# Optimization experiments

Hardware: AMD Instinct MI355X
Metric: run time of the kernel (lower is better)

## Reference

```python
import jax, jax.numpy as jnp
import numpy as np
from jax import lax

B, H, W = 8, 64, 64
D_IN, D_OUT, HEADS = 288, 576, 8
WIN, QS = 16, 2
MLP_H, BOT, NEXP = 4 * D_OUT, 32, 2
HEAD_DIM = D_OUT // HEADS


def _ln(x, g, b, eps=1e-6):
    m = jnp.mean(x, axis=-1, keepdims=True)
    v = jnp.var(x, axis=-1, keepdims=True)
    return (x - m) * lax.rsqrt(v + eps) * g + b


def _max_pool2(x):  # NHWC 2x2 max pool, stride 2
    return lax.reduce_window(x, -jnp.inf, lax.max, (1, 2, 2, 1), (1, 2, 2, 1), 'VALID')


def setup_inputs():
    key = jax.random.key(0)
    ks = iter(jax.random.split(key, 16))
    s = 0.02
    p = {}
    p['rgb'] = jax.random.normal(next(ks), (B, H, W, D_IN), jnp.float32)
    p['depth'] = jax.random.normal(next(ks), (B, H, W, D_IN), jnp.float32)
    p['norm1_g'] = jnp.ones((D_IN,), jnp.float32)
    p['norm1_b'] = jnp.zeros((D_IN,), jnp.float32)
    p['proj_w'] = jax.random.normal(next(ks), (D_IN, D_OUT), jnp.float32) * s
    p['proj_b'] = jnp.zeros((D_OUT,), jnp.float32)
    p['qkv_w'] = jax.random.normal(next(ks), (D_IN, 3 * D_OUT), jnp.float32) * s
    p['qkv_b'] = jnp.zeros((3 * D_OUT,), jnp.float32)
    p['attn_proj_w'] = jax.random.normal(next(ks), (D_OUT, D_OUT), jnp.float32) * s
    p['attn_proj_b'] = jnp.zeros((D_OUT,), jnp.float32)
    p['norm2_g'] = jnp.ones((D_OUT,), jnp.float32)
    p['norm2_b'] = jnp.zeros((D_OUT,), jnp.float32)
    p['mlp_w1'] = jax.random.normal(next(ks), (D_OUT, MLP_H), jnp.float32) * s
    p['mlp_b1'] = jnp.zeros((MLP_H,), jnp.float32)
    p['mlp_w2'] = jax.random.normal(next(ks), (MLP_H, D_OUT), jnp.float32) * s
    p['mlp_b2'] = jnp.zeros((D_OUT,), jnp.float32)
    # per-stream (rgb=0, depth=1) MoE adapters: 2 experts, bottleneck 32
    p['ad_gate_w'] = jax.random.normal(next(ks), (2, D_OUT, NEXP), jnp.float32) * s
    p['ad_gate_b'] = jnp.zeros((2, NEXP), jnp.float32)
    p['ad_down_w'] = jax.random.normal(next(ks), (2, NEXP, D_OUT, BOT), jnp.float32) * s
    p['ad_down_b'] = jnp.zeros((2, NEXP, BOT), jnp.float32)
    p['ad_up_w'] = jax.random.normal(next(ks), (2, NEXP, BOT, D_OUT), jnp.float32) * s
    p['ad_up_b'] = jnp.zeros((2, NEXP, D_OUT), jnp.float32)
    return p


def reference(rgb, depth, norm1_g, norm1_b, proj_w, proj_b, qkv_w, qkv_b,
              attn_proj_w, attn_proj_b, norm2_g, norm2_b,
              mlp_w1, mlp_b1, mlp_w2, mlp_b2,
              ad_gate_w, ad_gate_b, ad_down_w, ad_down_b, ad_up_w, ad_up_b):
    nW = H // WIN  # 4 windows per side (64 divisible by 16, no padding)
    w2 = WIN // QS  # pooled window side = 8

    def adapter(x, si):
        gate = jax.nn.softmax(x @ ad_gate_w[si] + ad_gate_b[si], axis=-1)  # [B,h,w,E]
        h = jax.nn.gelu(jnp.einsum('bhwd,edr->bhwer', x, ad_down_w[si]) + ad_down_b[si])
        y = jnp.einsum('bhwer,erd->bhwed', h, ad_up_w[si]) + ad_up_b[si]
        return 0.5 * jnp.sum(gate[..., None] * y, axis=-2)

    def stream(x, si):
        xn = _ln(x, norm1_g, norm1_b)
        # dim changes -> shortcut = do_pool(proj(norm1(x)))
        shortcut = _max_pool2(xn @ proj_w + proj_b)  # [B,32,32,576]
        xw = xn.reshape(B, nW, WIN, nW, WIN, D_IN).transpose(0, 1, 3, 2, 4, 5)
        xw = xw.reshape(B * nW * nW, WIN, WIN, D_IN)
        Bw = xw.shape[0]
        qkv = (xw.reshape(Bw, WIN * WIN, D_IN) @ qkv_w + qkv_b)
        qkv = qkv.reshape(Bw, WIN * WIN, 3, HEADS, HEAD_DIM)
        q, k, v = qkv[:, :, 0], qkv[:, :, 1], qkv[:, :, 2]
        # q-pool (2x2 max) inside each window
        q = _max_pool2(q.reshape(Bw, WIN, WIN, D_OUT)).reshape(Bw, w2 * w2, HEADS, HEAD_DIM)
        scale = 1.0 / np.sqrt(HEAD_DIM).astype(np.float32)
        attn = jax.nn.softmax(jnp.einsum('bqhd,bkhd->bhqk', q, k) * scale, axis=-1)
        o = jnp.einsum('bhqk,bkhd->bqhd', attn, v).reshape(Bw, w2, w2, D_OUT)
        o = o @ attn_proj_w + attn_proj_b
        # unpartition with pooled window size into 32x32
        o = o.reshape(B, nW, nW, w2, w2, D_OUT).transpose(0, 1, 3, 2, 4, 5)
        o = o.reshape(B, nW * w2, nW * w2, D_OUT)
        x = shortcut + o
        h = _ln(x, norm2_g, norm2_b)
        mlp = jax.nn.gelu(h @ mlp_w1 + mlp_b1) @ mlp_w2 + mlp_b2
        return x + mlp + adapter(x, si)

    return jnp.stack([stream(rgb, 0), stream(depth, 1)])  # [2,B,32,32,576]
```

## Files before the change

kernel.cpp:

```cpp
#include <hip/hip_runtime.h>
#include <cstdint>
#include <math.h>

typedef __bf16 bf16_t;
typedef __bf16 bf16x8 __attribute__((ext_vector_type(8)));
typedef float f32x4 __attribute__((ext_vector_type(4)));
typedef uint32_t u32x4 __attribute__((ext_vector_type(4)));
typedef uint32_t u32x2 __attribute__((ext_vector_type(2)));

#define DI __device__ __forceinline__

DI float bflo(uint32_t u){ return __builtin_bit_cast(float, (uint32_t)(u << 16)); }
DI float bfhi(uint32_t u){ return __builtin_bit_cast(float, (uint32_t)(u & 0xffff0000u)); }
DI uint16_t f2bf(float f){ bf16_t h = (bf16_t)f; return __builtin_bit_cast(uint16_t, h); }
DI uint32_t pk2(float a, float b){ return (uint32_t)f2bf(a) | ((uint32_t)f2bf(b) << 16); }
DI float geluf(float x){
  float u = 0.7978845608028654f * (x + 0.044715f * x * x * x);
  return 0.5f * x * (1.0f + tanhf(u));
}

#if defined(__has_builtin)
#if __has_builtin(__builtin_amdgcn_global_load_lds)
#define USE_GLLDS 1
#endif
#endif

#if USE_GLLDS
DI void gload_lds16(const void* g, void* l){
  __builtin_amdgcn_global_load_lds((__attribute__((address_space(1))) void*)g,
                                   (__attribute__((address_space(3))) void*)l, 16, 0, 0);
}
#endif

__global__ __launch_bounds__(256) void vtpad_k(uint16_t* __restrict__ vt)
{
  int idx = blockIdx.x * 256 + threadIdx.x;
  int wh = idx >> 11, r = (idx >> 8) & 7, c = idx & 255;
  vt[((size_t)(wh * 80 + 72 + r)) * 256 + c] = 0;
}

__global__ __launch_bounds__(256) void wtrans_k(const float* __restrict__ W, uint16_t* __restrict__ Wt,
                                                int K, int N, int Np, int ldw, int c0)
{
  int idx = blockIdx.x * 256 + threadIdx.x;
  if (idx >= Np * K) return;
  int n = idx / K, k = idx - n * K;
  float v = (n < N) ? W[(size_t)k * ldw + c0 + n] : 0.0f;
  Wt[idx] = f2bf(v);
}

__global__ __launch_bounds__(256) void mk_m2te_k(const float* __restrict__ w2,
    const float* __restrict__ uw, const float* __restrict__ ub, uint16_t* __restrict__ m2Te)
{
  int idx = blockIdx.x * 256 + threadIdx.x;
  if (idx >= 2 * 640 * 2400) return;
  int si = idx / (640 * 2400);
  int rem = idx - si * 640 * 2400;
  int n = rem / 2400, k = rem - n * 2400;
  float v = 0.0f;
  if (n < 576){
    if (k < 2304) v = w2[(size_t)k * 576 + n];
    else if (k < 2368){
      int e = (k - 2304) >> 5, r = (k - 2304) & 31;
      v = uw[((size_t)(si * 2 + e) * 32 + r) * 576 + n];
    } else if (k < 2370){
      v = ub[(size_t)(si * 2 + (k - 2368)) * 576 + n];
    }
  }
  m2Te[idx] = f2bf(v);
}

__global__ __launch_bounds__(256) void mk_adt_k(const float* __restrict__ dwn, const float* __restrict__ gw,
    const float* __restrict__ dbn, const float* __restrict__ gb,
    uint16_t* __restrict__ adT, float* __restrict__ adB)
{
  int idx = blockIdx.x * 256 + threadIdx.x;
  if (idx >= 2 * 128 * 576) return;
  int si = idx / (128 * 576);
  int rem = idx - si * 128 * 576;
  int n = rem / 576, k = rem - n * 576;
  float v = 0.0f;
  if (n < 64){
    int e = n >> 5, r = n & 31;
    v = dwn[((size_t)(si * 2 + e) * 576 + k) * 32 + r];
  } else if (n < 66){
    v = gw[(size_t)si * 1152 + k * 2 + (n - 64)];
  }
  adT[idx] = f2bf(v);
  if (k == 0){
    float bv = 0.0f;
    if (n < 64) bv = dbn[si * 64 + (n >> 5) * 32 + (n & 31)];
    else if (n < 66) bv = gb[si * 2 + (n - 64)];
    adB[si * 128 + n] = bv;
  }
}

__global__ __launch_bounds__(256) void mk_pqb_k(const float* __restrict__ pb, const float* __restrict__ qb,
                                                float* __restrict__ o)
{
  int i = blockIdx.x * 256 + threadIdx.x;
  if (i < 1280){
    float v = 0.0f;
    if (i < 576) v = pb[i];
    else if (i >= 640 && i < 1216) v = qb[i - 640];
    o[i] = v;
  }
}

__global__ __launch_bounds__(256) void ln_k(const float* __restrict__ in0, const int D,
                                            const float* __restrict__ g, const float* __restrict__ bb,
                                            uint16_t* __restrict__ outp)
{
  const int token = blockIdx.x * 4 + (threadIdx.x >> 6);
  const int lane = threadIdx.x & 63;
  const float* in = in0 + (size_t)token * D;
  const int nf4 = D >> 2;
  f32x4 v[3];
  float s = 0.f, sq = 0.f;
#pragma unroll
  for (int i = 0; i < 3; ++i){
    const int c = lane + 64 * i;
    if (c < nf4){
      v[i] = *(const f32x4*)(in + 4 * c);
#pragma unroll
      for (int e = 0; e < 4; ++e){ s += v[i][e]; sq += v[i][e] * v[i][e]; }
    }
  }
#pragma unroll
  for (int off = 32; off; off >>= 1){
    s  += __shfl_xor(s, off);
    sq += __shfl_xor(sq, off);
  }
  const float mean = s / (float)D;
  const float var = sq / (float)D - mean * mean;
  const float inv = rsqrtf(var + 1e-6f);
  uint16_t* orow = outp + (size_t)token * D;
#pragma unroll
  for (int i = 0; i < 3; ++i){
    const int c = lane + 64 * i;
    if (c < nf4){
      float f0 = (v[i][0] - mean) * inv * g[4*c+0] + bb[4*c+0];
      float f1 = (v[i][1] - mean) * inv * g[4*c+1] + bb[4*c+1];
      float f2 = (v[i][2] - mean) * inv * g[4*c+2] + bb[4*c+2];
      float f3 = (v[i][3] - mean) * inv * g[4*c+3] + bb[4*c+3];
      u32x2 pk; pk[0] = pk2(f0, f1); pk[1] = pk2(f2, f3);
      *(u32x2*)(orow + 4 * c) = pk;
    }
  }
}

template<int BM>
DI void gemm_core(const uint16_t* __restrict__ A, const uint16_t* __restrict__ Bt,
                  const int K, char* smem, const int tid, f32x4 (*acc)[4])
{
  constexpr int MI = BM / 32;
  constexpr int ABUF = BM * 64;
  char* A0 = smem;
  char* A1 = smem + ABUF;
  char* B0 = smem + 2 * ABUF;
  char* B1 = smem + 2 * ABUF + 8192;
  const int lane = tid & 63;
  const int wid = tid >> 6;
  const int wm = (wid >> 1) * (BM / 2);
  const int wn = (wid & 1) * 64;
  const int r15 = lane & 15, kh = lane >> 4;
  const int rA0 = tid >> 2, c16 = tid & 3;
  const int kS = ((c16 ^ ((rA0 >> 1) & 3)) << 3);

  auto stage = [&](char* Ad, char* Bd, int t){
    const uint16_t* ga0 = A + (size_t)rA0 * K + t * 32 + kS;
    const uint16_t* gb0 = Bt + (size_t)rA0 * K + t * 32 + kS;
    const uint16_t* gb1 = Bt + (size_t)(rA0 + 64) * K + t * 32 + kS;
#if USE_GLLDS
    gload_lds16(ga0, Ad + tid * 16);
    gload_lds16(gb0, Bd + tid * 16);
    gload_lds16(gb1, Bd + tid * 16 + 4096);
    if constexpr (BM == 128){
      const uint16_t* ga1 = A + (size_t)(rA0 + 64) * K + t * 32 + kS;
      gload_lds16(ga1, Ad + tid * 16 + 4096);
    }
#else
    *(u32x4*)(Ad + tid * 16)        = *(const u32x4*)ga0;
    *(u32x4*)(Bd + tid * 16)        = *(const u32x4*)gb0;
    *(u32x4*)(Bd + tid * 16 + 4096) = *(const u32x4*)gb1;
    if constexpr (BM == 128){
      const uint16_t* ga1 = A + (size_t)(rA0 + 64) * K + t * 32 + kS;
      *(u32x4*)(Ad + tid * 16 + 4096) = *(const u32x4*)ga1;
    }
#endif
  };

  stage(A0, B0, 0);
  __syncthreads();
  const int nt = K >> 5;
  for (int t = 0; t < nt; ++t){
    char* Ac = (t & 1) ? A1 : A0;
    char* Bc = (t & 1) ? B1 : B0;
    if (t + 1 < nt) stage((t & 1) ? A0 : A1, (t & 1) ? B0 : B1, t + 1);
    bf16x8 af[MI], bfv[4];
#pragma unroll
    for (int i = 0; i < MI; ++i){
      int rowA = wm + i * 16 + r15;
      af[i] = *(const bf16x8*)(Ac + rowA * 64 + ((kh ^ ((rowA >> 1) & 3)) << 4));
    }
#pragma unroll
    for (int j = 0; j < 4; ++j){
      int rowB = wn + j * 16 + r15;
      bfv[j] = *(const bf16x8*)(Bc + rowB * 64 + ((kh ^ ((rowB >> 1) & 3)) << 4));
    }
#pragma unroll
    for (int i = 0; i < MI; ++i)
#pragma unroll
      for (int j = 0; j < 4; ++j)
        acc[i][j] = __builtin_amdgcn_mfma_f32_16x16x32_bf16(af[i], bfv[j], acc[i][j], 0, 0, 0);
    __syncthreads();
  }
}

__global__ __launch_bounds__(256) void gemm_pkv_k(
    const uint16_t* __restrict__ xn, const uint16_t* __restrict__ pqT, const uint16_t* __restrict__ kvT,
    const float* __restrict__ pqB, const float* __restrict__ kvB,
    uint16_t* __restrict__ sc, uint16_t* __restrict__ qp,
    uint16_t* __restrict__ kb, uint16_t* __restrict__ vt)
{
  __shared__ __align__(16) char smem[32768];
  const int tid = threadIdx.x;
  const int m0 = blockIdx.x * 128;
  const int y = blockIdx.y;
  const bool pool = (y < 10);
  const int n0 = pool ? y * 128 : (y - 10) * 128;
  const uint16_t* Bt = (pool ? pqT : kvT) + (size_t)n0 * 288;
  f32x4 acc[4][4] = {};
  gemm_core<128>(xn + (size_t)m0 * 288, Bt, 288, smem, tid, acc);

  const int lane = tid & 63, wid = tid >> 6;
  const int wm = (wid >> 1) * 64, wn = (wid & 1) * 64;
  const int r15 = lane & 15, kh = lane >> 4;

  if (pool){
    uint16_t* Cp = (uint16_t*)smem;
#pragma unroll
    for (int i = 0; i < 4; ++i)
#pragma unroll
      for (int j = 0; j < 4; ++j)
#pragma unroll
        for (int tt = 0; tt < 4; ++tt){
          int rr2 = wm + i * 16 + kh * 4 + tt;
          int cc = wn + j * 16 + r15;
          Cp[rr2 * 128 + cc] = f2bf(acc[i][j][tt]);
        }
    __syncthreads();
    const int orow0 = m0 >> 2;
#pragma unroll
    for (int e2 = 0; e2 < 16; ++e2){
      int idx = tid + 256 * e2;
      int X = idx >> 7, c = idx & 127;
      int gn = n0 + c;
      if (gn < 1216){
        float v0 = bflo(Cp[(2 * X) * 128 + c]);
        float v1 = bflo(Cp[(2 * X + 1) * 128 + c]);
        float v2 = bflo(Cp[(64 + 2 * X) * 128 + c]);
        float v3 = bflo(Cp[(65 + 2 * X) * 128 + c]);
        float v = fmaxf(fmaxf(v0, v1), fmaxf(v2, v3)) + pqB[gn];
        if (gn < 576)
          sc[(size_t)(orow0 + X) * 576 + gn] = f2bf(v);
        else if (gn >= 640){
          int qn = gn - 640;
          if (qn < 576) qp[(size_t)(orow0 + X) * 576 + qn] = f2bf(v);
        }
      }
    }
  } else {
    int coln[4]; float bcol[4];
#pragma unroll
    for (int j = 0; j < 4; ++j){
      coln[j] = n0 + wn + j * 16 + r15;
      bcol[j] = kvB[coln[j]];
    }
#pragma unroll
    for (int i = 0; i < 4; ++i)
#pragma unroll
      for (int tt = 0; tt < 4; ++tt){
        const int gm = m0 + wm + i * 16 + kh * 4 + tt;
#pragma unroll
        for (int j = 0; j < 4; ++j){
          float v = acc[i][j][tt] + bcol[j];
          int n = coln[j];
          if (n < 576){
            kb[(size_t)gm * 576 + n] = f2bf(v);
          } else {
            int d = n - 576;
            int hh = d / 72, dd = d - hh * 72;
            int bimg = gm >> 12, yy = (gm >> 6) & 63, xx = gm & 63;
            int w = bimg * 16 + (yy >> 4) * 4 + (xx >> 4);
            int kl = (yy & 15) * 16 + (xx & 15);
            vt[((size_t)(w * 8 + hh) * 80 + dd) * 256 + kl] = f2bf(v);
          }
        }
      }
  }
}

__global__ __launch_bounds__(256) void gemm_add1_k(
    const uint16_t* __restrict__ ob, const uint16_t* __restrict__ aT, const float* __restrict__ bias,
    const uint16_t* __restrict__ sc, float* __restrict__ x2, uint16_t* __restrict__ x2b)
{
  __shared__ __align__(16) char smem[24576];
  const int tid = threadIdx.x;
  const int m0 = blockIdx.x * 64;
  const int n0 = blockIdx.y * 128;
  f32x4 acc[2][4] = {};
  gemm_core<64>(ob + (size_t)m0 * 576, aT + (size_t)n0 * 576, 576, smem, tid, acc);

  const int lane = tid & 63, wid = tid >> 6;
  const int wm = (wid >> 1) * 32, wn = (wid & 1) * 64;
  const int r15 = lane & 15, kh = lane >> 4;
  int coln[4]; float bcol[4];
#pragma unroll
  for (int j = 0; j < 4; ++j){
    coln[j] = n0 + wn + j * 16 + r15;
    bcol[j] = (coln[j] < 576) ? bias[coln[j]] : 0.0f;
  }
#pragma unroll
  for (int i = 0; i < 2; ++i)
#pragma unroll
    for (int tt = 0; tt < 4; ++tt){
      const int gm = m0 + wm + i * 16 + kh * 4 + tt;
      const size_t ro = (size_t)gm * 576;
#pragma unroll
      for (int j = 0; j < 4; ++j){
        if (coln[j] < 576){
          float v = acc[i][j][tt] + bcol[j] + bflo(sc[ro + coln[j]]);
          x2[ro + coln[j]] = v;
          x2b[ro + coln[j]] = f2bf(v);
        }
      }
    }
}

__global__ __launch_bounds__(256) void gemm_upad_k(
    const uint16_t* __restrict__ hb, const uint16_t* __restrict__ x2b,
    const uint16_t* __restrict__ m1T, const uint16_t* __restrict__ adT,
    const float* __restrict__ b1, const float* __restrict__ adB,
    uint16_t* __restrict__ mlpA)
{
  __shared__ __align__(16) char smem[24576];
  const int tid = threadIdx.x;
  const int m0 = blockIdx.x * 64;
  const int y = blockIdx.y;
  const bool up = (y < 18);
  const int n0 = up ? y * 128 : 0;
  const uint16_t* A = (up ? hb : x2b) + (size_t)m0 * 576;
  const uint16_t* Bt = up ? (m1T + (size_t)n0 * 576) : adT;
  f32x4 acc[2][4] = {};
  gemm_core<64>(A, Bt, 576, smem, tid, acc);

  const int lane = tid & 63, wid = tid >> 6;
  const int wm = (wid >> 1) * 32, wn = (wid & 1) * 64;
  const int r15 = lane & 15, kh = lane >> 4;

  if (up){
    const float* bias = b1;
#pragma unroll
    for (int i = 0; i < 2; ++i)
#pragma unroll
      for (int tt = 0; tt < 4; ++tt){
        const int gm = m0 + wm + i * 16 + kh * 4 + tt;
#pragma unroll
        for (int j = 0; j < 4; ++j){
          int c = n0 + wn + j * 16 + r15;
          float v = acc[i][j][tt] + bias[c];
          mlpA[(size_t)gm * 2400 + c] = f2bf(geluf(v));
        }
      }
  } else {
    float* gl = (float*)smem;
#pragma unroll
    for (int i = 0; i < 2; ++i)
#pragma unroll
      for (int j = 0; j < 4; ++j){
        int c = wn + j * 16 + r15;
        if (c == 64 || c == 65){
#pragma unroll
          for (int tt = 0; tt < 4; ++tt){
            int rr2 = wm + i * 16 + kh * 4 + tt;
            gl[rr2 * 2 + (c - 64)] = acc[i][j][tt] + adB[c];
          }
        }
      }
    __syncthreads();
#pragma unroll
    for (int i = 0; i < 2; ++i)
#pragma unroll
      for (int tt = 0; tt < 4; ++tt){
        int rr2 = wm + i * 16 + kh * 4 + tt;
        int gm = m0 + rr2;
        float l0 = gl[rr2 * 2], l1 = gl[rr2 * 2 + 1];
        float mx = fmaxf(l0, l1);
        float e0 = __expf(l0 - mx), e1 = __expf(l1 - mx);
        float inv = 0.5f / (e0 + e1);
#pragma unroll
        for (int j = 0; j < 4; ++j){
          int c = wn + j * 16 + r15;
          if (c < 96){
            float val;
            if (c < 64){
              float g = ((c >> 5) == 0 ? e0 : e1) * inv;
              val = g * geluf(acc[i][j][tt] + adB[c]);
            } else if (c == 64) val = e0 * inv;
            else if (c == 65) val = e1 * inv;
            else val = 0.0f;
            mlpA[(size_t)gm * 2400 + 2304 + c] = f2bf(val);
          }
        }
      }
  }
}

__global__ __launch_bounds__(256) void gemm_addf_k(
    const uint16_t* __restrict__ mlpA, const uint16_t* __restrict__ m2Te, const float* __restrict__ bias,
    const float* __restrict__ x2, float* __restrict__ outf)
{
  __shared__ __align__(16) char smem[24576];
  const int tid = threadIdx.x;
  const int m0 = blockIdx.x * 64;
  const int n0 = blockIdx.y * 128;
  f32x4 acc[2][4] = {};
  gemm_core<64>(mlpA + (size_t)m0 * 2400, m2Te + (size_t)n0 * 2400, 2400, smem, tid, acc);

  const int lane = tid & 63, wid = tid >> 6;
  const int wm = (wid >> 1) * 32, wn = (wid & 1) * 64;
  const int r15 = lane & 15, kh = lane >> 4;
  int coln[4]; float bcol[4];
#pragma unroll
  for (int j = 0; j < 4; ++j){
    coln[j] = n0 + wn + j * 16 + r15;
    bcol[j] = (coln[j] < 576) ? bias[coln[j]] : 0.0f;
  }
#pragma unroll
  for (int i = 0; i < 2; ++i)
#pragma unroll
    for (int tt = 0; tt < 4; ++tt){
      const int gm = m0 + wm + i * 16 + kh * 4 + tt;
      const size_t ro = (size_t)gm * 576;
#pragma unroll
      for (int j = 0; j < 4; ++j){
        if (coln[j] < 576){
          float v = acc[i][j][tt] + bcol[j] + x2[ro + coln[j]];
          outf[ro + coln[j]] = v;
        }
      }
    }
}

__global__ __launch_bounds__(64, 1) void attn_mfma_k(
    const uint16_t* __restrict__ qp,
    const uint16_t* __restrict__ kb,
    const uint16_t* __restrict__ vt,
    uint16_t* __restrict__ o)
{
  const int lane = threadIdx.x;
  const int r15 = lane & 15;
  const int kh = lane >> 4;
  const int bid = blockIdx.x;
  const int h = bid & 7;
  const int w = bid >> 3;
  const int b = w >> 4;
  const int wy = (w >> 2) & 3;
  const int wx = w & 3;

  const u32x4 ZU = {0, 0, 0, 0};
  const bf16x8 Z8 = __builtin_bit_cast(bf16x8, ZU);
  const float scale = 0.11785113019775793f;

  bf16x8 qf[4][3];
  int qrow[4];
#pragma unroll
  for (int j = 0; j < 4; ++j){
    int q = j * 16 + r15;
    int y = wy * 8 + (q >> 3), x = wx * 8 + (q & 7);
    qrow[j] = b * 1024 + y * 32 + x;
    const uint16_t* qpr = qp + (size_t)qrow[j] * 576 + h * 72;
    qf[j][0] = *(const bf16x8*)(qpr + kh * 8);
    qf[j][1] = *(const bf16x8*)(qpr + 32 + kh * 8);
    qf[j][2] = (kh == 0) ? *(const bf16x8*)(qpr + 64) : Z8;
  }

  float m[4], l[4];
#pragma unroll
  for (int j = 0; j < 4; ++j){ m[j] = -INFINITY; l[j] = 0.0f; }
  f32x4 acco[5][4] = {};
  const size_t vtbase = (size_t)(w * 8 + h) * 80 * 256;

  for (int t = 0; t < 4; ++t){
    f32x4 accs[4][4] = {};
#pragma unroll
    for (int i = 0; i < 4; ++i){
      const uint16_t* kr = kb + (size_t)(b * 4096 + (wy * 16 + t * 4 + i) * 64 + wx * 16 + r15) * 576 + h * 72;
      bf16x8 kf0 = *(const bf16x8*)(kr + kh * 8);
      bf16x8 kf1 = *(const bf16x8*)(kr + 32 + kh * 8);
      bf16x8 kf2 = (kh == 0) ? *(const bf16x8*)(kr + 64) : Z8;
#pragma unroll
      for (int j = 0; j < 4; ++j){
        accs[i][j] = __builtin_amdgcn_mfma_f32_16x16x32_bf16(kf0, qf[j][0], accs[i][j], 0, 0, 0);
        accs[i][j] = __builtin_amdgcn_mfma_f32_16x16x32_bf16(kf1, qf[j][1], accs[i][j], 0, 0, 0);
        accs[i][j] = __builtin_amdgcn_mfma_f32_16x16x32_bf16(kf2, qf[j][2], accs[i][j], 0, 0, 0);
      }
    }
#pragma unroll
    for (int j = 0; j < 4; ++j){
      float mx = -INFINITY;
#pragma unroll
      for (int i = 0; i < 4; ++i)
#pragma unroll
        for (int tt = 0; tt < 4; ++tt){
          float sv = accs[i][j][tt] * scale;
          accs[i][j][tt] = sv;
          mx = fmaxf(mx, sv);
        }
      mx = fmaxf(mx, __shfl_xor(mx, 16));
      mx = fmaxf(mx, __shfl_xor(mx, 32));
      float nm = fmaxf(m[j], mx);
      float f = __expf(m[j] - nm);
      m[j] = nm;
      l[j] *= f;
#pragma unroll
      for (int i2 = 0; i2 < 5; ++i2) acco[i2][j] *= f;
      float ls = 0.0f;
#pragma unroll
      for (int i = 0; i < 4; ++i)
#pragma unroll
        for (int tt = 0; tt < 4; ++tt){
          float p = __expf(accs[i][j][tt] - nm);
          accs[i][j][tt] = p;
          ls += p;
        }
      ls += __shfl_xor(ls, 16);
      ls += __shfl_xor(ls, 32);
      l[j] += ls;
    }
    uint32_t pw[4][4][2];
#pragma unroll
    for (int i = 0; i < 4; ++i)
#pragma unroll
      for (int j = 0; j < 4; ++j){
        pw[i][j][0] = pk2(accs[i][j][0], accs[i][j][1]);
        pw[i][j][1] = pk2(accs[i][j][2], accs[i][j][3]);
      }
#pragma unroll
    for (int ks = 0; ks < 2; ++ks){
      bf16x8 pb[4];
#pragma unroll
      for (int j = 0; j < 4; ++j){
        u32x4 u = {pw[2 * ks][j][0], pw[2 * ks][j][1], pw[2 * ks + 1][j][0], pw[2 * ks + 1][j][1]};
        pb[j] = __builtin_bit_cast(bf16x8, u);
      }
#pragma unroll
      for (int i2 = 0; i2 < 5; ++i2){
        const uint16_t* vr = vt + vtbase + (size_t)(i2 * 16 + r15) * 256 + t * 64 + ks * 32 + kh * 4;
        u32x2 lo = *(const u32x2*)(vr);
        u32x2 hi = *(const u32x2*)(vr + 16);
        u32x4 av = {lo[0], lo[1], hi[0], hi[1]};
        bf16x8 va = __builtin_bit_cast(bf16x8, av);
#pragma unroll
        for (int j = 0; j < 4; ++j)
          acco[i2][j] = __builtin_amdgcn_mfma_f32_16x16x32_bf16(va, pb[j], acco[i2][j], 0, 0, 0);
      }
    }
  }

#pragma unroll
  for (int j = 0; j < 4; ++j){
    float inv = 1.0f / l[j];
    uint16_t* orow = o + (size_t)qrow[j] * 576 + h * 72;
#pragma unroll
    for (int i2 = 0; i2 < 5; ++i2)
#pragma unroll
      for (int tt = 0; tt < 4; ++tt){
        int d = i2 * 16 + kh * 4 + tt;
        if (d < 72) orow[d] = f2bf(acco[i2][j][tt] * inv);
      }
  }
}

extern "C" void kernel_launch(void* const* d_in, const int* in_sizes, int n_in,
                              void* d_out, int out_size, void* d_ws, size_t ws_size,
                              hipStream_t stream)
{
  (void)in_sizes; (void)n_in; (void)out_size; (void)ws_size;
  const float* srcs[2] = { (const float*)d_in[0], (const float*)d_in[1] };
  const float* n1g    = (const float*)d_in[2];
  const float* n1b    = (const float*)d_in[3];
  const float* proj_w = (const float*)d_in[4];
  const float* proj_b = (const float*)d_in[5];
  const float* qkv_w  = (const float*)d_in[6];
  const float* qkv_b  = (const float*)d_in[7];
  const float* ap_w   = (const float*)d_in[8];
  const float* ap_b   = (const float*)d_in[9];
  const float* n2g    = (const float*)d_in[10];
  const float* n2b    = (const float*)d_in[11];
  const float* w1     = (const float*)d_in[12];
  const float* b1     = (const float*)d_in[13];
  const float* w2     = (const float*)d_in[14];
  const float* b2     = (const float*)d_in[15];
  const float* gw     = (const float*)d_in[16];
  const float* gb     = (const float*)d_in[17];
  const float* dwn    = (const float*)d_in[18];
  const float* dbn    = (const float*)d_in[19];
  const float* uw     = (const float*)d_in[20];
  const float* ub     = (const float*)d_in[21];

  char* ws = (char*)d_ws;
  size_t off = 0;
  auto alloc = [&](size_t bytes){ size_t o = off; off += (bytes + 255) & ~(size_t)255; return o; };

  uint16_t* pqT   = (uint16_t*)(ws + alloc((size_t)1280 * 288 * 2));
  float*    pqB   = (float*)(ws + alloc((size_t)1280 * 4));
  uint16_t* kvT   = (uint16_t*)(ws + alloc((size_t)1152 * 288 * 2));
  uint16_t* aT    = (uint16_t*)(ws + alloc((size_t)640 * 576 * 2));
  uint16_t* m1T   = (uint16_t*)(ws + alloc((size_t)2304 * 576 * 2));
  uint16_t* m2Te  = (uint16_t*)(ws + alloc((size_t)2 * 640 * 2400 * 2));
  uint16_t* adT   = (uint16_t*)(ws + alloc((size_t)2 * 128 * 576 * 2));
  float*    adB   = (float*)(ws + alloc((size_t)2 * 128 * 4));
  size_t oXN = alloc((size_t)32768 * 288 * 2);
  uint16_t* xn  = (uint16_t*)(ws + oXN);
  float*    x2  = (float*)(ws + oXN);
  uint16_t* sc  = (uint16_t*)(ws + alloc((size_t)8192 * 576 * 2));
  size_t oQP = alloc((size_t)8192 * 576 * 2);
  uint16_t* qp  = (uint16_t*)(ws + oQP);
  uint16_t* x2b = (uint16_t*)(ws + oQP);
  uint16_t* kb  = (uint16_t*)(ws + alloc((size_t)32768 * 576 * 2));
  size_t oVT = alloc((size_t)1024 * 80 * 256 * 2);
  uint16_t* vt   = (uint16_t*)(ws + oVT);
  uint16_t* mlpA = (uint16_t*)(ws + oVT);
  size_t oR2 = alloc((size_t)2 * 8192 * 576 * 2);
  uint16_t* ob = (uint16_t*)(ws + oR2);
  uint16_t* hb = (uint16_t*)(ws + oR2 + (size_t)8192 * 576 * 2);

  wtrans_k<<<(640 * 288 + 255) / 256, 256, 0, stream>>>(proj_w, pqT, 288, 576, 640, 576, 0);
  wtrans_k<<<(640 * 288 + 255) / 256, 256, 0, stream>>>(qkv_w, pqT + (size_t)640 * 288, 288, 576, 640, 1728, 0);
  mk_pqb_k<<<5, 256, 0, stream>>>(proj_b, qkv_b, pqB);
  wtrans_k<<<(1152 * 288 + 255) / 256, 256, 0, stream>>>(qkv_w, kvT, 288, 1152, 1152, 1728, 576);
  wtrans_k<<<(640 * 576 + 255) / 256, 256, 0, stream>>>(ap_w, aT, 576, 576, 640, 576, 0);
  wtrans_k<<<(2304 * 576 + 255) / 256, 256, 0, stream>>>(w1, m1T, 576, 2304, 2304, 2304, 0);
  mk_m2te_k<<<(2 * 640 * 2400 + 255) / 256, 256, 0, stream>>>(w2, uw, ub, m2Te);
  mk_adt_k<<<(2 * 128 * 576 + 255) / 256, 256, 0, stream>>>(dwn, gw, dbn, gb, adT, adB);

  for (int si = 0; si < 2; ++si){
    float* outf = (float*)d_out + (size_t)si * 8192 * 576;

    ln_k<<<8192, 256, 0, stream>>>(srcs[si], 288, n1g, n1b, xn);

    vtpad_k<<<(1024 * 8 * 256) / 256, 256, 0, stream>>>(vt);

    gemm_pkv_k<<<dim3(256, 19), 256, 0, stream>>>(xn, pqT, kvT, pqB, qkv_b + 576, sc, qp, kb, vt);

    attn_mfma_k<<<1024, 64, 0, stream>>>(qp, kb, vt, ob);

    gemm_add1_k<<<dim3(128, 5), 256, 0, stream>>>(ob, aT, ap_b, sc, x2, x2b);

    ln_k<<<2048, 256, 0, stream>>>(x2, 576, n2g, n2b, hb);

    gemm_upad_k<<<dim3(128, 19), 256, 0, stream>>>(hb, x2b, m1T, adT + (size_t)si * 128 * 576,
                                                   b1, adB + si * 128, mlpA);

    gemm_addf_k<<<dim3(128, 5), 256, 0, stream>>>(mlpA, m2Te + (size_t)si * 640 * 2400, b2, x2, outf);
  }
}
```

Baseline: 652.1 us.

## Pack proj/q weights densely and preload full K into LDS in pkv GEMM

Removes the padding between the proj and q weight blocks (640 to 576 rows each), so the pooled GEMM needs 9 instead of 10 column tiles and the grid drops from 19 to 18 column blocks. The pkv GEMM now loads the entire K=288 slab of A and B into 144KB of shared memory up front, waits once, then runs all MFMAs without per-step barriers. The epilogue staging buffer also gets a padded row stride of 136 to reduce LDS bank conflicts. The large LDS footprint limits occupancy to one block per CU and removes any overlap between loads and compute inside a block.

```diff
diff --git a/kernel.cpp b/kernel.cpp
--- a/kernel.cpp
+++ b/kernel.cpp
@@ -99,12 +99,7 @@
                                                 float* __restrict__ o)
 {
   int i = blockIdx.x * 256 + threadIdx.x;
-  if (i < 1280){
-    float v = 0.0f;
-    if (i < 576) v = pb[i];
-    else if (i >= 640 && i < 1216) v = qb[i - 640];
-    o[i] = v;
-  }
+  if (i < 1152) o[i] = (i < 576) ? pb[i] : qb[i - 576];
 }
 
 __global__ __launch_bounds__(256) void ln_k(const float* __restrict__ in0, const int D,
@@ -223,19 +218,70 @@
     uint16_t* __restrict__ sc, uint16_t* __restrict__ qp,
     uint16_t* __restrict__ kb, uint16_t* __restrict__ vt)
 {
-  __shared__ __align__(16) char smem[32768];
+  __shared__ __align__(16) char smem[147456];
   const int tid = threadIdx.x;
   const int m0 = blockIdx.x * 128;
   const int y = blockIdx.y;
-  const bool pool = (y < 10);
-  const int n0 = pool ? y * 128 : (y - 10) * 128;
+  const bool pool = (y < 9);
+  const int n0 = pool ? y * 128 : (y - 9) * 128;
+  const uint16_t* A = xn + (size_t)m0 * 288;
   const uint16_t* Bt = (pool ? pqT : kvT) + (size_t)n0 * 288;
+
+  const int lane = tid & 63;
+  const int wid = tid >> 6;
+  const int wm = (wid >> 1) * 64;
+  const int wn = (wid & 1) * 64;
+  const int r15 = lane & 15, kh = lane >> 4;
+  const int rA0 = tid >> 2, c16 = tid & 3;
+  const int kS = ((c16 ^ ((rA0 >> 1) & 3)) << 3);
+
+  char* As = smem;
+  char* Bs = smem + 73728;
+#pragma unroll
+  for (int t = 0; t < 9; ++t){
+#if USE_GLLDS
+    gload_lds16(A  + (size_t)rA0 * 288 + t * 32 + kS,        As + t * 8192 + tid * 16);
+    gload_lds16(A  + (size_t)(rA0 + 64) * 288 + t * 32 + kS, As + t * 8192 + 4096 + tid * 16);
+    gload_lds16(Bt + (size_t)rA0 * 288 + t * 32 + kS,        Bs + t * 8192 + tid * 16);
+    gload_lds16(Bt + (size_t)(rA0 + 64) * 288 + t * 32 + kS, Bs + t * 8192 + 4096 + tid * 16);
+#else
+    *(u32x4*)(As + t * 8192 + tid * 16)        = *(const u32x4*)(A  + (size_t)rA0 * 288 + t * 32 + kS);
+    *(u32x4*)(As + t * 8192 + 4096 + tid * 16) = *(const u32x4*)(A  + (size_t)(rA0 + 64) * 288 + t * 32 + kS);
+    *(u32x4*)(Bs + t * 8192 + tid * 16)        = *(const u32x4*)(Bt + (size_t)rA0 * 288 + t * 32 + kS);
+    *(u32x4*)(Bs + t * 8192 + 4096 + tid * 16) = *(const u32x4*)(Bt + (size_t)(rA0 + 64) * 288 + t * 32 + kS);
+#endif
+  }
+#if USE_GLLDS
+  asm volatile("s_waitcnt vmcnt(0)" ::: "memory");
+  __builtin_amdgcn_s_barrier();
+  __builtin_amdgcn_sched_barrier(0);
+#else
+  __syncthreads();
+#endif
+
   f32x4 acc[4][4] = {};
-  gemm_core<128>(xn + (size_t)m0 * 288, Bt, 288, smem, tid, acc);
-
-  const int lane = tid & 63, wid = tid >> 6;
-  const int wm = (wid >> 1) * 64, wn = (wid & 1) * 64;
-  const int r15 = lane & 15, kh = lane >> 4;
+#pragma unroll
+  for (int t = 0; t < 9; ++t){
+    const char* Ac = As + t * 8192;
+    const char* Bc = Bs + t * 8192;
+    bf16x8 af[4], bfv[4];
+#pragma unroll
+    for (int i = 0; i < 4; ++i){
+      int rowA = wm + i * 16 + r15;
+      af[i] = *(const bf16x8*)(Ac + rowA * 64 + ((kh ^ ((rowA >> 1) & 3)) << 4));
+    }
+#pragma unroll
+    for (int j = 0; j < 4; ++j){
+      int rowB = wn + j * 16 + r15;
+      bfv[j] = *(const bf16x8*)(Bc + rowB * 64 + ((kh ^ ((rowB >> 1) & 3)) << 4));
+    }
+#pragma unroll
+    for (int i = 0; i < 4; ++i)
+#pragma unroll
+      for (int j = 0; j < 4; ++j)
+        acc[i][j] = __builtin_amdgcn_mfma_f32_16x16x32_bf16(af[i], bfv[j], acc[i][j], 0, 0, 0);
+  }
+  __syncthreads();
 
   if (pool){
     uint16_t* Cp = (uint16_t*)smem;
@@ -247,7 +293,7 @@
         for (int tt = 0; tt < 4; ++tt){
           int rr2 = wm + i * 16 + kh * 4 + tt;
           int cc = wn + j * 16 + r15;
-          Cp[rr2 * 128 + cc] = f2bf(acc[i][j][tt]);
+          Cp[rr2 * 136 + cc] = f2bf(acc[i][j][tt]);
         }
     __syncthreads();
     const int orow0 = m0 >> 2;
@@ -256,19 +302,15 @@
       int idx = tid + 256 * e2;
       int X = idx >> 7, c = idx & 127;
       int gn = n0 + c;
-      if (gn < 1216){
-        float v0 = bflo(Cp[(2 * X) * 128 + c]);
-        float v1 = bflo(Cp[(2 * X + 1) * 128 + c]);
-        float v2 = bflo(Cp[(64 + 2 * X) * 128 + c]);
-        float v3 = bflo(Cp[(65 + 2 * X) * 128 + c]);
-        float v = fmaxf(fmaxf(v0, v1), fmaxf(v2, v3)) + pqB[gn];
-        if (gn < 576)
-          sc[(size_t)(orow0 + X) * 576 + gn] = f2bf(v);
-        else if (gn >= 640){
-          int qn = gn - 640;
-          if (qn < 576) qp[(size_t)(orow0 + X) * 576 + qn] = f2bf(v);
-        }
-      }
+      float v0 = bflo(Cp[(2 * X) * 136 + c]);
+      float v1 = bflo(Cp[(2 * X + 1) * 136 + c]);
+      float v2 = bflo(Cp[(64 + 2 * X) * 136 + c]);
+      float v3 = bflo(Cp[(65 + 2 * X) * 136 + c]);
+      float v = fmaxf(fmaxf(v0, v1), fmaxf(v2, v3)) + pqB[gn];
+      if (gn < 576)
+        sc[(size_t)(orow0 + X) * 576 + gn] = f2bf(v);
+      else
+        qp[(size_t)(orow0 + X) * 576 + (gn - 576)] = f2bf(v);
     }
   } else {
     int coln[4]; float bcol[4];
@@ -614,8 +656,8 @@
   size_t off = 0;
   auto alloc = [&](size_t bytes){ size_t o = off; off += (bytes + 255) & ~(size_t)255; return o; };
 
-  uint16_t* pqT   = (uint16_t*)(ws + alloc((size_t)1280 * 288 * 2));
-  float*    pqB   = (float*)(ws + alloc((size_t)1280 * 4));
+  uint16_t* pqT   = (uint16_t*)(ws + alloc((size_t)1152 * 288 * 2));
+  float*    pqB   = (float*)(ws + alloc((size_t)1152 * 4));
   uint16_t* kvT   = (uint16_t*)(ws + alloc((size_t)1152 * 288 * 2));
   uint16_t* aT    = (uint16_t*)(ws + alloc((size_t)640 * 576 * 2));
   uint16_t* m1T   = (uint16_t*)(ws + alloc((size_t)2304 * 576 * 2));
@@ -637,8 +679,8 @@
   uint16_t* ob = (uint16_t*)(ws + oR2);
   uint16_t* hb = (uint16_t*)(ws + oR2 + (size_t)8192 * 576 * 2);
 
-  wtrans_k<<<(640 * 288 + 255) / 256, 256, 0, stream>>>(proj_w, pqT, 288, 576, 640, 576, 0);
-  wtrans_k<<<(640 * 288 + 255) / 256, 256, 0, stream>>>(qkv_w, pqT + (size_t)640 * 288, 288, 576, 640, 1728, 0);
+  wtrans_k<<<(576 * 288 + 255) / 256, 256, 0, stream>>>(proj_w, pqT, 288, 576, 576, 576, 0);
+  wtrans_k<<<(576 * 288 + 255) / 256, 256, 0, stream>>>(qkv_w, pqT + (size_t)576 * 288, 288, 576, 576, 1728, 0);
   mk_pqb_k<<<5, 256, 0, stream>>>(proj_b, qkv_b, pqB);
   wtrans_k<<<(1152 * 288 + 255) / 256, 256, 0, stream>>>(qkv_w, kvT, 288, 1152, 1152, 1728, 576);
   wtrans_k<<<(640 * 576 + 255) / 256, 256, 0, stream>>>(ap_w, aT, 576, 576, 640, 576, 0);
@@ -653,7 +695,7 @@
 
     vtpad_k<<<(1024 * 8 * 256) / 256, 256, 0, stream>>>(vt);
 
-    gemm_pkv_k<<<dim3(256, 19), 256, 0, stream>>>(xn, pqT, kvT, pqB, qkv_b + 576, sc, qp, kb, vt);
+    gemm_pkv_k<<<dim3(256, 18), 256, 0, stream>>>(xn, pqT, kvT, pqB, qkv_b + 576, sc, qp, kb, vt);
 
     attn_mfma_k<<<1024, 64, 0, stream>>>(qp, kb, vt, ob);
 
```

Measured after the change: 751.5 us. 15.2% more time.
